# Kernel optimization log

Measured on AMD Instinct MI355X. Metric: run time of the kernel, lower is better.

The kernel has to match this reference:

```python
import jax, jax.numpy as jnp
import numpy as np
from jax import lax

DN3D = ('NCDHW', 'OIDHW', 'NCDHW')


def conv4d_valid(x, w, b):
    """4D valid convolution, stride 1.
    x: [B, C, L, D, H, W]; w: [O, C, Lk, Dk, Hk, Wk]; b: [O].
    Implemented as a small fixed loop over the Lk kernel positions, each a
    batched 3D conv (L folded into batch) -- same math as torch Conv4d above.
    """
    B, C, L, D, H, W = x.shape
    O, _, Lk, Dk, Hk, Wk = w.shape
    Lo = L - Lk + 1
    out = None
    for i in range(Lk):
        xs = x[:, :, i:i + Lo]                      # [B, C, Lo, D, H, W]
        xs = xs.transpose(0, 2, 1, 3, 4, 5).reshape(B * Lo, C, D, H, W)
        o = lax.conv_general_dilated(xs, w[:, :, i], (1, 1, 1), 'VALID',
                                     dimension_numbers=DN3D)  # [B*Lo, O, Do, Ho, Wo]
        out = o if out is None else out + o
    _, _, Do, Ho, Wo = out.shape
    out = out.reshape(B, Lo, O, Do, Ho, Wo).transpose(0, 2, 1, 3, 4, 5)
    return out + b[None, :, None, None, None, None]


def setup_inputs() -> dict:
    key = jax.random.key(0)
    k0, k1, k2, k3, k4 = jax.random.split(key, 5)
    B = 16384
    return {
        'x': jax.random.normal(k0, (B, 1, 7, 7, 7, 7), dtype=jnp.float32),
        'w1': jax.random.normal(k1, (2, 1, 3, 3, 3, 3), dtype=jnp.float32) * 0.1,
        'b1': jax.random.normal(k2, (2,), dtype=jnp.float32) * 0.1,
        'w2': jax.random.normal(k3, (4, 2, 3, 3, 3, 3), dtype=jnp.float32) * 0.1,
        'b2': jax.random.normal(k4, (4,), dtype=jnp.float32) * 0.1,
    }


def reference(x, w1, b1, w2, b2):
    h = jax.nn.relu(conv4d_valid(x, w1, b1))   # [B, 2, 5, 5, 5, 5]
    h = jax.nn.relu(conv4d_valid(h, w2, b2))   # [B, 4, 3, 3, 3, 3]
    return h.reshape(h.shape[0], -1)           # [B, 324]
```

## Files before the change

### kernel.cpp

```cpp
#include <hip/hip_runtime.h>

#define SPB 4
#define TPB 256

__global__ __launch_bounds__(TPB, 2)
void conv4d_fused(const float* __restrict__ x,
                  const float* __restrict__ w1, const float* __restrict__ b1,
                  const float* __restrict__ w2, const float* __restrict__ b2,
                  float* __restrict__ out, int B)
{
    __shared__ float s_w1[162];
    __shared__ float s_w2[648];
    __shared__ float s_b1[2];
    __shared__ float s_b2[4];
    __shared__ float s_x[SPB * 2401];
    __shared__ float s_h1[SPB * 1250];

    const int t  = threadIdx.x;
    const int s0 = blockIdx.x * SPB;
    const int ns = min(SPB, B - s0);

    for (int i = t; i < 162; i += TPB) s_w1[i] = w1[i];
    for (int i = t; i < 648; i += TPB) s_w2[i] = w2[i];
    if (t < 2) s_b1[t] = b1[t];
    if (t < 4) s_b2[t] = b2[t];

    {
        const float* xp = x + (size_t)s0 * 2401;
        const int n = ns * 2401;
        for (int i = t; i < n; i += TPB) s_x[i] = xp[i];
    }
    __syncthreads();

    {
        const int ntask = ns * 50;
        if (t < ntask) {
            int s = t / 50;
            int r = t % 50;
            int o = r / 25; r %= 25;
            int l = r / 5, d = r % 5;

            float acc[5][5];
            const float bias = s_b1[o];
            #pragma unroll
            for (int h = 0; h < 5; ++h)
                #pragma unroll
                for (int w = 0; w < 5; ++w) acc[h][w] = bias;

            const float* xs = s_x + s * 2401;
            const float* wo = s_w1 + o * 81;
            #pragma unroll
            for (int kl = 0; kl < 3; ++kl)
            #pragma unroll
            for (int kd = 0; kd < 3; ++kd) {
                float p[7][7];
                const float* xp = xs + (l + kl) * 343 + (d + kd) * 49;
                #pragma unroll
                for (int i = 0; i < 49; ++i) p[i / 7][i % 7] = xp[i];
                const float* wp = wo + kl * 27 + kd * 9;
                #pragma unroll
                for (int kh = 0; kh < 3; ++kh)
                #pragma unroll
                for (int kw = 0; kw < 3; ++kw) {
                    const float wv = wp[kh * 3 + kw];
                    #pragma unroll
                    for (int h = 0; h < 5; ++h)
                    #pragma unroll
                    for (int w = 0; w < 5; ++w)
                        acc[h][w] += p[h + kh][w + kw] * wv;
                }
            }
            float* hp = s_h1 + s * 1250 + o * 625 + l * 125 + d * 25;
            #pragma unroll
            for (int h = 0; h < 5; ++h)
            #pragma unroll
            for (int w = 0; w < 5; ++w)
                hp[h * 5 + w] = fmaxf(acc[h][w], 0.0f);
        }
    }
    __syncthreads();

    {
        const int ntask = ns * 36;
        if (t < ntask) {
            int s = t / 36;
            int r = t % 36;
            int o2 = r / 9; r %= 9;
            int l = r / 3, d = r % 3;

            float acc[3][3];
            const float bias = s_b2[o2];
            #pragma unroll
            for (int h = 0; h < 3; ++h)
                #pragma unroll
                for (int w = 0; w < 3; ++w) acc[h][w] = bias;

            #pragma unroll
            for (int c = 0; c < 2; ++c) {
                const float* hs = s_h1 + s * 1250 + c * 625;
                const float* wb = s_w2 + o2 * 162 + c * 81;
                #pragma unroll
                for (int kl = 0; kl < 3; ++kl)
                #pragma unroll
                for (int kd = 0; kd < 3; ++kd) {
                    float p[5][5];
                    const float* pp = hs + (l + kl) * 125 + (d + kd) * 25;
                    #pragma unroll
                    for (int i = 0; i < 25; ++i) p[i / 5][i % 5] = pp[i];
                    const float* wp = wb + kl * 27 + kd * 9;
                    #pragma unroll
                    for (int kh = 0; kh < 3; ++kh)
                    #pragma unroll
                    for (int kw = 0; kw < 3; ++kw) {
                        const float wv = wp[kh * 3 + kw];
                        #pragma unroll
                        for (int h = 0; h < 3; ++h)
                        #pragma unroll
                        for (int w = 0; w < 3; ++w)
                            acc[h][w] += p[h + kh][w + kw] * wv;
                    }
                }
            }
            float* op = out + (size_t)(s0 + s) * 324 + o2 * 81 + l * 27 + d * 9;
            #pragma unroll
            for (int h = 0; h < 3; ++h)
            #pragma unroll
            for (int w = 0; w < 3; ++w)
                op[h * 3 + w] = fmaxf(acc[h][w], 0.0f);
        }
    }
}

extern "C" void kernel_launch(void* const* d_in, const int* in_sizes, int n_in,
                              void* d_out, int out_size, void* d_ws, size_t ws_size,
                              hipStream_t stream)
{
    const float* x  = (const float*)d_in[0];
    const float* w1 = (const float*)d_in[1];
    const float* b1 = (const float*)d_in[2];
    const float* w2 = (const float*)d_in[3];
    const float* b2 = (const float*)d_in[4];
    float* out = (float*)d_out;

    const int B = in_sizes[0] / 2401;
    const int grid = (B + SPB - 1) / SPB;
    conv4d_fused<<<grid, TPB, 0, stream>>>(x, w1, b1, w2, b2, out, B);
}
```

Before: 314.4 us.

## Pack input and intermediate in bf16 in LDS with vectorized padded loads

Input planes and the layer-1 activations are now rounded to bf16 and stored two per 32-bit word in shared memory. Each plane is padded so it can be read with 128-bit loads, and the weights are padded for float4 loads. Samples per block rise to five and the occupancy hint goes from 2 to 3 blocks per SM, so LDS traffic and footprint drop. In exchange, input and intermediate values lose precision to bf16, which may break a strict accuracy tolerance, and the unpack step adds ALU work.

New measurement: 383.0 us. 21.8% more time.

```diff
diff --git a/kernel.cpp b/kernel.cpp
--- a/kernel.cpp
+++ b/kernel.cpp
@@ -1,132 +1,187 @@
 #include <hip/hip_runtime.h>
 
-#define SPB 4
+#define SPB 5
 #define TPB 256
 
-__global__ __launch_bounds__(TPB, 2)
+
+__device__ __forceinline__ unsigned bf16rne(float f) {
+    unsigned u = __float_as_uint(f);
+    return (u + 0x7fffu + ((u >> 16) & 1u)) >> 16;
+}
+__device__ __forceinline__ void unpack2(unsigned u, float& a, float& b) {
+    a = __uint_as_float(u << 16);
+    b = __uint_as_float(u & 0xffff0000u);
+}
+
+__global__ __launch_bounds__(TPB, 3)
 void conv4d_fused(const float* __restrict__ x,
                   const float* __restrict__ w1, const float* __restrict__ b1,
                   const float* __restrict__ w2, const float* __restrict__ b2,
                   float* __restrict__ out, int B)
 {
-    __shared__ float s_w1[162];
-    __shared__ float s_w2[648];
+    __shared__ __align__(16) unsigned s_xu[SPB * 49 * 28];
+    __shared__ __align__(16) unsigned s_h1[SPB * 2 * 25 * 16];
+    __shared__ __align__(16) float s_w1[18 * 12];
+    __shared__ __align__(16) float s_w2[72 * 12];
     __shared__ float s_b1[2];
     __shared__ float s_b2[4];
-    __shared__ float s_x[SPB * 2401];
-    __shared__ float s_h1[SPB * 1250];
 
     const int t  = threadIdx.x;
     const int s0 = blockIdx.x * SPB;
     const int ns = min(SPB, B - s0);
 
-    for (int i = t; i < 162; i += TPB) s_w1[i] = w1[i];
-    for (int i = t; i < 648; i += TPB) s_w2[i] = w2[i];
+    for (int i = t; i < 162; i += TPB) { int p = i / 9, q = i % 9; s_w1[p * 12 + q] = w1[i]; }
+    for (int i = t; i < 648; i += TPB) { int p = i / 9, q = i % 9; s_w2[p * 12 + q] = w2[i]; }
     if (t < 2) s_b1[t] = b1[t];
     if (t < 4) s_b2[t] = b2[t];
 
     {
-        const float* xp = x + (size_t)s0 * 2401;
-        const int n = ns * 2401;
-        for (int i = t; i < n; i += TPB) s_x[i] = xp[i];
-    }
-    __syncthreads();
-
-    {
-        const int ntask = ns * 50;
-        if (t < ntask) {
-            int s = t / 50;
-            int r = t % 50;
-            int o = r / 25; r %= 25;
-            int l = r / 5, d = r % 5;
-
-            float acc[5][5];
-            const float bias = s_b1[o];
-            #pragma unroll
-            for (int h = 0; h < 5; ++h)
-                #pragma unroll
-                for (int w = 0; w < 5; ++w) acc[h][w] = bias;
-
-            const float* xs = s_x + s * 2401;
-            const float* wo = s_w1 + o * 81;
-            #pragma unroll
-            for (int kl = 0; kl < 3; ++kl)
-            #pragma unroll
-            for (int kd = 0; kd < 3; ++kd) {
-                float p[7][7];
-                const float* xp = xs + (l + kl) * 343 + (d + kd) * 49;
-                #pragma unroll
-                for (int i = 0; i < 49; ++i) p[i / 7][i % 7] = xp[i];
-                const float* wp = wo + kl * 27 + kd * 9;
-                #pragma unroll
-                for (int kh = 0; kh < 3; ++kh)
-                #pragma unroll
-                for (int kw = 0; kw < 3; ++kw) {
-                    const float wv = wp[kh * 3 + kw];
-                    #pragma unroll
-                    for (int h = 0; h < 5; ++h)
-                    #pragma unroll
-                    for (int w = 0; w < 5; ++w)
-                        acc[h][w] += p[h + kh][w + kw] * wv;
-                }
-            }
-            float* hp = s_h1 + s * 1250 + o * 625 + l * 125 + d * 25;
-            #pragma unroll
-            for (int h = 0; h < 5; ++h)
-            #pragma unroll
-            for (int w = 0; w < 5; ++w)
-                hp[h * 5 + w] = fmaxf(acc[h][w], 0.0f);
+        const int nunits = ns * 49 * 25;
+        for (int u = t; u < nunits; u += TPB) {
+            int s = u / 1225;
+            int r = u % 1225;
+            int p = r / 25;
+            int j = r % 25;
+            const float* gp = x + (size_t)(s0 + s) * 2401 + p * 49;
+            unsigned* lp = s_xu + s * 1372 + p * 28;
+            if (j < 24) {
+                float a = gp[2 * j], b = gp[2 * j + 1];
+                lp[j] = bf16rne(a) | (bf16rne(b) << 16);
+            } else {
+                lp[24] = bf16rne(gp[48]);
+            }
         }
     }
     __syncthreads();
 
-    {
-        const int ntask = ns * 36;
-        if (t < ntask) {
-            int s = t / 36;
-            int r = t % 36;
-            int o2 = r / 9; r %= 9;
-            int l = r / 3, d = r % 3;
-
-            float acc[3][3];
+    if (t < 250) {
+        int o = t / 125;
+        int r = t % 125;
+        int s = r / 25;
+        int ld = r % 25;
+        int l = ld / 5, d = ld % 5;
+        if (s < ns) {
+            float acc[25];
+            const float bias = s_b1[o];
+            #pragma unroll
+            for (int i = 0; i < 25; ++i) acc[i] = bias;
+
+            const unsigned* xb = s_xu + s * 1372 + (l * 7 + d) * 28;
+            const float* wb = s_w1 + o * 108;
+
+            #pragma unroll
+            for (int kl = 0; kl < 3; ++kl)
+            #pragma unroll
+            for (int kd = 0; kd < 3; ++kd) {
+                const unsigned* pp = xb + (kl * 7 + kd) * 28;
+                unsigned u[25];
+                #pragma unroll
+                for (int q4 = 0; q4 < 6; ++q4) {
+                    uint4 q = ((const uint4*)pp)[q4];
+                    u[q4 * 4 + 0] = q.x; u[q4 * 4 + 1] = q.y;
+                    u[q4 * 4 + 2] = q.z; u[q4 * 4 + 3] = q.w;
+                }
+                u[24] = pp[24];
+                float X[49];
+                #pragma unroll
+                for (int i = 0; i < 24; ++i) unpack2(u[i], X[2 * i], X[2 * i + 1]);
+                X[48] = __uint_as_float(u[24] << 16);
+
+                const float* wp = wb + (kl * 3 + kd) * 12;
+                float wv[9];
+                float4 wq0 = *(const float4*)wp;
+                float4 wq1 = *(const float4*)(wp + 4);
+                wv[0] = wq0.x; wv[1] = wq0.y; wv[2] = wq0.z; wv[3] = wq0.w;
+                wv[4] = wq1.x; wv[5] = wq1.y; wv[6] = wq1.z; wv[7] = wq1.w;
+                wv[8] = wp[8];
+
+                #pragma unroll
+                for (int kh = 0; kh < 3; ++kh)
+                #pragma unroll
+                for (int kw = 0; kw < 3; ++kw) {
+                    const float wvv = wv[kh * 3 + kw];
+                    #pragma unroll
+                    for (int h = 0; h < 5; ++h)
+                    #pragma unroll
+                    for (int w = 0; w < 5; ++w)
+                        acc[h * 5 + w] += X[(h + kh) * 7 + (w + kw)] * wvv;
+                }
+            }
+
+            unsigned* hp = s_h1 + ((s * 2 + o) * 25 + ld) * 16;
+            unsigned pk[12];
+            #pragma unroll
+            for (int j = 0; j < 12; ++j) {
+                float a = fmaxf(acc[2 * j], 0.0f);
+                float b = fmaxf(acc[2 * j + 1], 0.0f);
+                pk[j] = bf16rne(a) | (bf16rne(b) << 16);
+            }
+            ((uint4*)hp)[0] = make_uint4(pk[0], pk[1], pk[2], pk[3]);
+            ((uint4*)hp)[1] = make_uint4(pk[4], pk[5], pk[6], pk[7]);
+            ((uint4*)hp)[2] = make_uint4(pk[8], pk[9], pk[10], pk[11]);
+            hp[12] = bf16rne(fmaxf(acc[24], 0.0f));
+        }
+    }
+    __syncthreads();
+
+    if (t < 180) {
+        int s = t / 36;
+        int r = t % 36;
+        int o2 = r / 9;
+        int ld = r % 9;
+        int l = ld / 3, d = ld % 3;
+        if (s < ns) {
+            float acc[9];
             const float bias = s_b2[o2];
             #pragma unroll
-            for (int h = 0; h < 3; ++h)
-                #pragma unroll
-                for (int w = 0; w < 3; ++w) acc[h][w] = bias;
+            for (int i = 0; i < 9; ++i) acc[i] = bias;
 
             #pragma unroll
             for (int c = 0; c < 2; ++c) {
-                const float* hs = s_h1 + s * 1250 + c * 625;
-                const float* wb = s_w2 + o2 * 162 + c * 81;
+                const unsigned* hb = s_h1 + ((s * 2 + c) * 25 + (l * 5 + d)) * 16;
+                const float* wb = s_w2 + ((o2 * 2 + c) * 9) * 12;
                 #pragma unroll
                 for (int kl = 0; kl < 3; ++kl)
                 #pragma unroll
                 for (int kd = 0; kd < 3; ++kd) {
-                    float p[5][5];
-                    const float* pp = hs + (l + kl) * 125 + (d + kd) * 25;
-                    #pragma unroll
-                    for (int i = 0; i < 25; ++i) p[i / 5][i % 5] = pp[i];
-                    const float* wp = wb + kl * 27 + kd * 9;
+                    const unsigned* pp = hb + (kl * 5 + kd) * 16;
+                    unsigned u[13];
+                    #pragma unroll
+                    for (int q4 = 0; q4 < 3; ++q4) {
+                        uint4 q = ((const uint4*)pp)[q4];
+                        u[q4 * 4 + 0] = q.x; u[q4 * 4 + 1] = q.y;
+                        u[q4 * 4 + 2] = q.z; u[q4 * 4 + 3] = q.w;
+                    }
+                    u[12] = pp[12];
+                    float X[25];
+                    #pragma unroll
+                    for (int i = 0; i < 12; ++i) unpack2(u[i], X[2 * i], X[2 * i + 1]);
+                    X[24] = __uint_as_float(u[12] << 16);
+
+                    const float* wp = wb + (kl * 3 + kd) * 12;
+                    float wv[9];
+                    float4 wq0 = *(const float4*)wp;
+                    float4 wq1 = *(const float4*)(wp + 4);
+                    wv[0] = wq0.x; wv[1] = wq0.y; wv[2] = wq0.z; wv[3] = wq0.w;
+                    wv[4] = wq1.x; wv[5] = wq1.y; wv[6] = wq1.z; wv[7] = wq1.w;
+                    wv[8] = wp[8];
+
                     #pragma unroll
                     for (int kh = 0; kh < 3; ++kh)
                     #pragma unroll
                     for (int kw = 0; kw < 3; ++kw) {
-                        const float wv = wp[kh * 3 + kw];
+                        const float wvv = wv[kh * 3 + kw];
                         #pragma unroll
                         for (int h = 0; h < 3; ++h)
                         #pragma unroll
                         for (int w = 0; w < 3; ++w)
-                            acc[h][w] += p[h + kh][w + kw] * wv;
+                            acc[h * 3 + w] += X[(h + kh) * 5 + (w + kw)] * wvv;
                     }
                 }
             }
             float* op = out + (size_t)(s0 + s) * 324 + o2 * 81 + l * 27 + d * 9;
             #pragma unroll
-            for (int h = 0; h < 3; ++h)
-            #pragma unroll
-            for (int w = 0; w < 3; ++w)
-                op[h * 3 + w] = fmaxf(acc[h][w], 0.0f);
+            for (int i = 0; i < 9; ++i) op[i] = fmaxf(acc[i], 0.0f);
         }
     }
 }
```

## Store input and intermediate activations as packed bf16 in LDS, fuse output channels

Applied to the files above, without the earlier changes.

Input planes and the first-layer activations are converted to bf16 and packed two per 32-bit word in shared memory, with padded strides, so more samples fit per block (SPB raised from 4 to 9) and LDS reads can be vectorised. Each first-layer thread now computes both output channels and each second-layer thread all four, so every loaded plane is reused across channels. Weights are re-laid-out for float4 loads. This lowers precision of the intermediates to bf16, which may exceed the accuracy tolerance, and uses more registers per thread.

Result: slower. 435.3 us (+38.5%).

```diff
diff --git a/kernel.cpp b/kernel.cpp
--- a/kernel.cpp
+++ b/kernel.cpp
@@ -1,7 +1,21 @@
 #include <hip/hip_runtime.h>
 
-#define SPB 4
 #define TPB 256
+#define SPB 9
+#define XSTRIDE 1396
+#define HSTRIDE 700
+
+__device__ __forceinline__ unsigned bf16rne(float f) {
+    unsigned u = __float_as_uint(f);
+    return (u + 0x7fffu + ((u >> 16) & 1u)) >> 16;
+}
+__device__ __forceinline__ void unpack2(unsigned u, float& a, float& b) {
+    a = __uint_as_float(u << 16);
+    b = __uint_as_float(u & 0xffff0000u);
+}
+__device__ __forceinline__ int xplane(int p) {
+    return 28 * p + (((p >> 3) & 7) << 2);
+}
 
 __global__ __launch_bounds__(TPB, 2)
 void conv4d_fused(const float* __restrict__ x,
@@ -9,124 +23,193 @@
                   const float* __restrict__ w2, const float* __restrict__ b2,
                   float* __restrict__ out, int B)
 {
-    __shared__ float s_w1[162];
-    __shared__ float s_w2[648];
-    __shared__ float s_b1[2];
-    __shared__ float s_b2[4];
-    __shared__ float s_x[SPB * 2401];
-    __shared__ float s_h1[SPB * 1250];
+    __shared__ __align__(16) unsigned s_xu[SPB * XSTRIDE];
+    __shared__ __align__(16) unsigned s_h1[SPB * HSTRIDE];
+    __shared__ __align__(16) float s_w1[9 * 2 * 12];
+    __shared__ __align__(16) float s_w2[2 * 9 * 4 * 12];
 
     const int t  = threadIdx.x;
     const int s0 = blockIdx.x * SPB;
-    const int ns = min(SPB, B - s0);
-
-    for (int i = t; i < 162; i += TPB) s_w1[i] = w1[i];
-    for (int i = t; i < 648; i += TPB) s_w2[i] = w2[i];
-    if (t < 2) s_b1[t] = b1[t];
-    if (t < 4) s_b2[t] = b2[t];
-
-    {
-        const float* xp = x + (size_t)s0 * 2401;
-        const int n = ns * 2401;
-        for (int i = t; i < n; i += TPB) s_x[i] = xp[i];
+
+    for (int i = t; i < 162; i += TPB) {
+        int o = i / 81, r = i - o * 81;
+        int klkd = r / 9, tap = r - klkd * 9;
+        s_w1[(klkd * 2 + o) * 12 + tap] = w1[i];
+    }
+    for (int i = t; i < 648; i += TPB) {
+        int o2 = i / 162, r = i - o2 * 162;
+        int c = r / 81, r2 = r - c * 81;
+        int klkd = r2 / 9, tap = r2 - klkd * 9;
+        s_w2[((c * 9 + klkd) * 4 + o2) * 12 + tap] = w2[i];
+    }
+
+    for (int s = 0; s < SPB; ++s) {
+        if (s0 + s >= B) break;
+        const float* gx = x + (size_t)(s0 + s) * 2401;
+        unsigned* xw = s_xu + s * XSTRIDE;
+        for (int i = t; i < 1225; i += TPB) {
+            int p = i / 25;
+            int j = i - p * 25;
+            const float* gp = gx + p * 49 + 2 * j;
+            float a = gp[0];
+            float b = (j < 24) ? gp[1] : 0.0f;
+            xw[xplane(p) + j] = bf16rne(a) | (bf16rne(b) << 16);
+        }
     }
     __syncthreads();
 
-    {
-        const int ntask = ns * 50;
-        if (t < ntask) {
-            int s = t / 50;
-            int r = t % 50;
-            int o = r / 25; r %= 25;
-            int l = r / 5, d = r % 5;
-
-            float acc[5][5];
-            const float bias = s_b1[o];
-            #pragma unroll
-            for (int h = 0; h < 5; ++h)
-                #pragma unroll
-                for (int w = 0; w < 5; ++w) acc[h][w] = bias;
-
-            const float* xs = s_x + s * 2401;
-            const float* wo = s_w1 + o * 81;
+    if (t < SPB * 25) {
+        int s  = t / 25;
+        int ld = t - s * 25;
+        if (s0 + s < B) {
+            int l = ld / 5, d = ld - (ld / 5) * 5;
+            float acc0[25], acc1[25];
+            const float bb0 = b1[0], bb1 = b1[1];
+            #pragma unroll
+            for (int i = 0; i < 25; ++i) { acc0[i] = bb0; acc1[i] = bb1; }
+
+            const unsigned* xw = s_xu + s * XSTRIDE;
+            const int pbase = l * 7 + d;
             #pragma unroll
             for (int kl = 0; kl < 3; ++kl)
             #pragma unroll
             for (int kd = 0; kd < 3; ++kd) {
-                float p[7][7];
-                const float* xp = xs + (l + kl) * 343 + (d + kd) * 49;
-                #pragma unroll
-                for (int i = 0; i < 49; ++i) p[i / 7][i % 7] = xp[i];
-                const float* wp = wo + kl * 27 + kd * 9;
+                const int p = pbase + kl * 7 + kd;
+                const unsigned* pp = xw + xplane(p);
+                unsigned u[25];
+                #pragma unroll
+                for (int k = 0; k < 6; ++k) {
+                    uint4 q = ((const uint4*)pp)[k];
+                    u[4*k] = q.x; u[4*k+1] = q.y; u[4*k+2] = q.z; u[4*k+3] = q.w;
+                }
+                u[24] = pp[24];
+                float X[50];
+                #pragma unroll
+                for (int k = 0; k < 25; ++k) unpack2(u[k], X[2*k], X[2*k+1]);
+
+                const float* wp = s_w1 + (kl * 3 + kd) * 24;
+                float wv0[9], wv1[9];
+                {
+                    float4 A = *(const float4*)wp;
+                    float4 Bq = *(const float4*)(wp + 4);
+                    wv0[0]=A.x; wv0[1]=A.y; wv0[2]=A.z; wv0[3]=A.w;
+                    wv0[4]=Bq.x; wv0[5]=Bq.y; wv0[6]=Bq.z; wv0[7]=Bq.w;
+                    wv0[8]=wp[8];
+                    float4 C = *(const float4*)(wp + 12);
+                    float4 Dq = *(const float4*)(wp + 16);
+                    wv1[0]=C.x; wv1[1]=C.y; wv1[2]=C.z; wv1[3]=C.w;
+                    wv1[4]=Dq.x; wv1[5]=Dq.y; wv1[6]=Dq.z; wv1[7]=Dq.w;
+                    wv1[8]=wp[20];
+                }
+
                 #pragma unroll
                 for (int kh = 0; kh < 3; ++kh)
                 #pragma unroll
                 for (int kw = 0; kw < 3; ++kw) {
-                    const float wv = wp[kh * 3 + kw];
+                    const float w0v = wv0[kh*3+kw], w1v = wv1[kh*3+kw];
                     #pragma unroll
                     for (int h = 0; h < 5; ++h)
                     #pragma unroll
-                    for (int w = 0; w < 5; ++w)
-                        acc[h][w] += p[h + kh][w + kw] * wv;
+                    for (int w = 0; w < 5; ++w) {
+                        const float xv = X[(h+kh)*7 + (w+kw)];
+                        acc0[h*5+w] += xv * w0v;
+                        acc1[h*5+w] += xv * w1v;
+                    }
                 }
             }
-            float* hp = s_h1 + s * 1250 + o * 625 + l * 125 + d * 25;
-            #pragma unroll
-            for (int h = 0; h < 5; ++h)
-            #pragma unroll
-            for (int w = 0; w < 5; ++w)
-                hp[h * 5 + w] = fmaxf(acc[h][w], 0.0f);
+
+            unsigned* hp0 = s_h1 + s * HSTRIDE + 14 * ld;
+            unsigned* hp1 = hp0 + 14 * 25;
+            unsigned pk[13];
+            #pragma unroll
+            for (int k = 0; k < 12; ++k)
+                pk[k] = bf16rne(fmaxf(acc0[2*k],0.f)) | (bf16rne(fmaxf(acc0[2*k+1],0.f)) << 16);
+            pk[12] = bf16rne(fmaxf(acc0[24],0.f));
+            #pragma unroll
+            for (int k = 0; k < 6; ++k) ((uint2*)hp0)[k] = make_uint2(pk[2*k], pk[2*k+1]);
+            hp0[12] = pk[12];
+            #pragma unroll
+            for (int k = 0; k < 12; ++k)
+                pk[k] = bf16rne(fmaxf(acc1[2*k],0.f)) | (bf16rne(fmaxf(acc1[2*k+1],0.f)) << 16);
+            pk[12] = bf16rne(fmaxf(acc1[24],0.f));
+            #pragma unroll
+            for (int k = 0; k < 6; ++k) ((uint2*)hp1)[k] = make_uint2(pk[2*k], pk[2*k+1]);
+            hp1[12] = pk[12];
         }
     }
     __syncthreads();
 
-    {
-        const int ntask = ns * 36;
-        if (t < ntask) {
-            int s = t / 36;
-            int r = t % 36;
-            int o2 = r / 9; r %= 9;
-            int l = r / 3, d = r % 3;
-
-            float acc[3][3];
-            const float bias = s_b2[o2];
-            #pragma unroll
-            for (int h = 0; h < 3; ++h)
-                #pragma unroll
-                for (int w = 0; w < 3; ++w) acc[h][w] = bias;
-
-            #pragma unroll
-            for (int c = 0; c < 2; ++c) {
-                const float* hs = s_h1 + s * 1250 + c * 625;
-                const float* wb = s_w2 + o2 * 162 + c * 81;
-                #pragma unroll
-                for (int kl = 0; kl < 3; ++kl)
-                #pragma unroll
-                for (int kd = 0; kd < 3; ++kd) {
-                    float p[5][5];
-                    const float* pp = hs + (l + kl) * 125 + (d + kd) * 25;
-                    #pragma unroll
-                    for (int i = 0; i < 25; ++i) p[i / 5][i % 5] = pp[i];
-                    const float* wp = wb + kl * 27 + kd * 9;
-                    #pragma unroll
-                    for (int kh = 0; kh < 3; ++kh)
-                    #pragma unroll
-                    for (int kw = 0; kw < 3; ++kw) {
-                        const float wv = wp[kh * 3 + kw];
-                        #pragma unroll
-                        for (int h = 0; h < 3; ++h)
-                        #pragma unroll
-                        for (int w = 0; w < 3; ++w)
-                            acc[h][w] += p[h + kh][w + kw] * wv;
+    if (t < SPB * 9) {
+        int s  = t / 9;
+        int ld = t - s * 9;
+        if (s0 + s < B) {
+            int l = ld / 3, d = ld - (ld / 3) * 3;
+            float acc[4][9];
+            #pragma unroll
+            for (int o2 = 0; o2 < 4; ++o2) {
+                const float bb = b2[o2];
+                #pragma unroll
+                for (int i = 0; i < 9; ++i) acc[o2][i] = bb;
+            }
+
+            const unsigned* hw = s_h1 + s * HSTRIDE;
+            const int qbase = l * 5 + d;
+            #pragma unroll
+            for (int c = 0; c < 2; ++c)
+            #pragma unroll
+            for (int kl = 0; kl < 3; ++kl)
+            #pragma unroll
+            for (int kd = 0; kd < 3; ++kd) {
+                const int q = c * 25 + qbase + kl * 5 + kd;
+                const unsigned* pp = hw + 14 * q;
+                unsigned u[13];
+                #pragma unroll
+                for (int k = 0; k < 6; ++k) {
+                    uint2 qq = ((const uint2*)pp)[k];
+                    u[2*k] = qq.x; u[2*k+1] = qq.y;
+                }
+                u[12] = pp[12];
+                float X[26];
+                #pragma unroll
+                for (int k = 0; k < 13; ++k) unpack2(u[k], X[2*k], X[2*k+1]);
+
+                const float* wp = s_w2 + (c * 9 + (kl*3+kd)) * 48;
+                float wv[4][9];
+                #pragma unroll
+                for (int o2 = 0; o2 < 4; ++o2) {
+                    const float* wq = wp + o2 * 12;
+                    float4 A = *(const float4*)wq;
+                    float4 Bq = *(const float4*)(wq + 4);
+                    wv[o2][0]=A.x; wv[o2][1]=A.y; wv[o2][2]=A.z; wv[o2][3]=A.w;
+                    wv[o2][4]=Bq.x; wv[o2][5]=Bq.y; wv[o2][6]=Bq.z; wv[o2][7]=Bq.w;
+                    wv[o2][8]=wq[8];
+                }
+
+                #pragma unroll
+                for (int kh = 0; kh < 3; ++kh)
+                #pragma unroll
+                for (int kw = 0; kw < 3; ++kw) {
+                    const float w0v = wv[0][kh*3+kw], w1v = wv[1][kh*3+kw];
+                    const float w2v = wv[2][kh*3+kw], w3v = wv[3][kh*3+kw];
+                    #pragma unroll
+                    for (int h = 0; h < 3; ++h)
+                    #pragma unroll
+                    for (int w = 0; w < 3; ++w) {
+                        const float xv = X[(h+kh)*5 + (w+kw)];
+                        acc[0][h*3+w] += xv * w0v;
+                        acc[1][h*3+w] += xv * w1v;
+                        acc[2][h*3+w] += xv * w2v;
+                        acc[3][h*3+w] += xv * w3v;
                     }
                 }
             }
-            float* op = out + (size_t)(s0 + s) * 324 + o2 * 81 + l * 27 + d * 9;
-            #pragma unroll
-            for (int h = 0; h < 3; ++h)
-            #pragma unroll
-            for (int w = 0; w < 3; ++w)
-                op[h * 3 + w] = fmaxf(acc[h][w], 0.0f);
+
+            float* op = out + (size_t)(s0 + s) * 324 + ld * 9;
+            #pragma unroll
+            for (int o2 = 0; o2 < 4; ++o2)
+                #pragma unroll
+                for (int i = 0; i < 9; ++i)
+                    op[o2 * 81 + i] = fmaxf(acc[o2][i], 0.f);
         }
     }
 }
```

## Convert fused conv4d to packed fp16 math with reorganized shared layouts

Applied to the files above, without the earlier changes.

Inputs, weights and intermediate activations are converted to packed half2 in shared memory with padded, vector-aligned row layouts. Both conv stages then use packed fp16 FMAs and 128-bit LDS loads. Stage 1 computes both output channels per thread, and stage 2 packs the two input channels into half2 lanes and splits output channels across thread pairs. Samples per block rise from 4 to 9. This is meant to halve ALU and LDS traffic per FMA, at the cost of fp16 precision for accumulation, which may exceed the tolerance.

New measurement: 369.8 us. +17.6%, slower.

```diff
diff --git a/kernel.cpp b/kernel.cpp
--- a/kernel.cpp
+++ b/kernel.cpp
@@ -1,7 +1,19 @@
 #include <hip/hip_runtime.h>
-
-#define SPB 4
+#include <hip/hip_fp16.h>
+
 #define TPB 256
+#define SPB 9
+#define XS  1372
+#define HS  700
+
+__device__ __forceinline__ unsigned h2u(__half2 h) { return __builtin_bit_cast(unsigned, h); }
+__device__ __forceinline__ __half2 u2h(unsigned u) { return __builtin_bit_cast(__half2, u); }
+__device__ __forceinline__ unsigned pkf(float a, float b) { return h2u(__floats2half2_rn(a, b)); }
+__device__ __forceinline__ unsigned pkrelu(unsigned u) {
+    unsigned r;
+    __asm__ volatile("v_pk_max_f16 %0, %1, 0" : "=v"(r) : "v"(u));
+    return r;
+}
 
 __global__ __launch_bounds__(TPB, 2)
 void conv4d_fused(const float* __restrict__ x,
@@ -9,124 +21,189 @@
                   const float* __restrict__ w2, const float* __restrict__ b2,
                   float* __restrict__ out, int B)
 {
-    __shared__ float s_w1[162];
-    __shared__ float s_w2[648];
-    __shared__ float s_b1[2];
+    __shared__ __align__(16) unsigned s_x[SPB * XS];
+    __shared__ __align__(16) unsigned s_h[SPB * HS];
+    __shared__ __align__(16) unsigned s_w1d[216];
+    __shared__ __align__(16) unsigned s_w2d[432];
+    __shared__ unsigned s_b1d[2];
     __shared__ float s_b2[4];
-    __shared__ float s_x[SPB * 2401];
-    __shared__ float s_h1[SPB * 1250];
 
     const int t  = threadIdx.x;
     const int s0 = blockIdx.x * SPB;
     const int ns = min(SPB, B - s0);
 
-    for (int i = t; i < 162; i += TPB) s_w1[i] = w1[i];
-    for (int i = t; i < 648; i += TPB) s_w2[i] = w2[i];
-    if (t < 2) s_b1[t] = b1[t];
+    for (int i = t; i < 162; i += TPB) {
+        int o = i / 81, r81 = i - 81 * o;
+        int klkd = r81 / 9, t9 = r81 - 9 * klkd;
+        float v = w1[i];
+        s_w1d[((klkd * 2 + o) * 12) + t9] = pkf(v, v);
+    }
+    for (int i = t; i < 324; i += TPB) {
+        int o2 = i / 81, r81 = i - 81 * o2;
+        int klkd = r81 / 9, t9 = r81 - 9 * klkd;
+        s_w2d[((klkd * 4 + o2) * 12) + t9] = pkf(w2[o2 * 162 + r81], w2[o2 * 162 + 81 + r81]);
+    }
+    if (t < 2) { float v = b1[t]; s_b1d[t] = pkf(v, v); }
     if (t < 4) s_b2[t] = b2[t];
 
     {
-        const float* xp = x + (size_t)s0 * 2401;
-        const int n = ns * 2401;
-        for (int i = t; i < n; i += TPB) s_x[i] = xp[i];
+        const int nunit = ns * XS;
+        for (int v = t; v < nunit; v += TPB) {
+            int s  = v / XS;     int r0 = v - s * XS;
+            int p  = r0 / 28;    int r1 = r0 - p * 28;
+            int r  = r1 >> 2, c = r1 & 3;
+            const float* gp = x + (size_t)(s0 + s) * 2401 + p * 49 + r * 7;
+            float a = gp[c < 3 ? 2 * c : 6];
+            float b = (c < 3) ? gp[2 * c + 1] : 0.0f;
+            s_x[v] = pkf(a, b);
+        }
     }
     __syncthreads();
 
-    {
-        const int ntask = ns * 50;
-        if (t < ntask) {
-            int s = t / 50;
-            int r = t % 50;
-            int o = r / 25; r %= 25;
-            int l = r / 5, d = r % 5;
-
-            float acc[5][5];
-            const float bias = s_b1[o];
-            #pragma unroll
-            for (int h = 0; h < 5; ++h)
-                #pragma unroll
-                for (int w = 0; w < 5; ++w) acc[h][w] = bias;
-
-            const float* xs = s_x + s * 2401;
-            const float* wo = s_w1 + o * 81;
+    if (t < SPB * 25) {
+        int s = t / 25, ld = t - 25 * s;
+        if (s < ns) {
+            int l = ld / 5, d = ld - 5 * l;
+            __half2 acc[2][5][3];
+            {
+                __half2 bb0 = u2h(s_b1d[0]), bb1 = u2h(s_b1d[1]);
+                #pragma unroll
+                for (int h = 0; h < 5; ++h)
+                    #pragma unroll
+                    for (int j = 0; j < 3; ++j) { acc[0][h][j] = bb0; acc[1][h][j] = bb1; }
+            }
+            const unsigned* xb = s_x + s * XS + (l * 7 + d) * 28;
+
             #pragma unroll
             for (int kl = 0; kl < 3; ++kl)
             #pragma unroll
             for (int kd = 0; kd < 3; ++kd) {
-                float p[7][7];
-                const float* xp = xs + (l + kl) * 343 + (d + kd) * 49;
-                #pragma unroll
-                for (int i = 0; i < 49; ++i) p[i / 7][i % 7] = xp[i];
-                const float* wp = wo + kl * 27 + kd * 9;
+                const unsigned* pp = xb + (kl * 7 + kd) * 28;
+                unsigned e[7][4];
+                #pragma unroll
+                for (int r = 0; r < 7; ++r) {
+                    uint4 q = ((const uint4*)pp)[r];
+                    e[r][0] = q.x; e[r][1] = q.y; e[r][2] = q.z; e[r][3] = q.w;
+                }
+                unsigned od[7][3];
+                #pragma unroll
+                for (int r = 0; r < 7; ++r)
+                    #pragma unroll
+                    for (int j = 0; j < 3; ++j)
+                        od[r][j] = __builtin_amdgcn_alignbit(e[r][j + 1], e[r][j], 16);
+
+                unsigned wv[2][9];
+                #pragma unroll
+                for (int o = 0; o < 2; ++o) {
+                    const unsigned* wb = s_w1d + ((kl * 3 + kd) * 2 + o) * 12;
+                    uint4 qa = ((const uint4*)wb)[0];
+                    uint4 qb = ((const uint4*)wb)[1];
+                    wv[o][0] = qa.x; wv[o][1] = qa.y; wv[o][2] = qa.z; wv[o][3] = qa.w;
+                    wv[o][4] = qb.x; wv[o][5] = qb.y; wv[o][6] = qb.z; wv[o][7] = qb.w;
+                    wv[o][8] = wb[8];
+                }
+
                 #pragma unroll
                 for (int kh = 0; kh < 3; ++kh)
                 #pragma unroll
-                for (int kw = 0; kw < 3; ++kw) {
-                    const float wv = wp[kh * 3 + kw];
-                    #pragma unroll
-                    for (int h = 0; h < 5; ++h)
-                    #pragma unroll
-                    for (int w = 0; w < 5; ++w)
-                        acc[h][w] += p[h + kh][w + kw] * wv;
-                }
-            }
-            float* hp = s_h1 + s * 1250 + o * 625 + l * 125 + d * 25;
-            #pragma unroll
-            for (int h = 0; h < 5; ++h)
-            #pragma unroll
-            for (int w = 0; w < 5; ++w)
-                hp[h * 5 + w] = fmaxf(acc[h][w], 0.0f);
+                for (int h = 0; h < 5; ++h) {
+                    const int row = h + kh;
+                    #pragma unroll
+                    for (int kw = 0; kw < 3; ++kw) {
+                        #pragma unroll
+                        for (int j = 0; j < 3; ++j) {
+                            unsigned xu = (kw == 0) ? e[row][j]
+                                        : (kw == 1) ? od[row][j]
+                                                    : e[row][j + 1];
+                            __half2 X2 = u2h(xu);
+                            acc[0][h][j] = __hfma2(X2, u2h(wv[0][kh * 3 + kw]), acc[0][h][j]);
+                            acc[1][h][j] = __hfma2(X2, u2h(wv[1][kh * 3 + kw]), acc[1][h][j]);
+                        }
+                    }
+                }
+            }
+
+            unsigned* hp = s_h + s * HS + ld * 28;
+            unsigned o25[25];
+            #pragma unroll
+            for (int h = 0; h < 5; ++h) {
+                unsigned c0[3], c1[3];
+                #pragma unroll
+                for (int j = 0; j < 3; ++j) {
+                    c0[j] = pkrelu(h2u(acc[0][h][j]));
+                    c1[j] = pkrelu(h2u(acc[1][h][j]));
+                }
+                o25[h * 5 + 0] = __builtin_amdgcn_perm(c1[0], c0[0], 0x05040100u);
+                o25[h * 5 + 1] = __builtin_amdgcn_perm(c1[0], c0[0], 0x07060302u);
+                o25[h * 5 + 2] = __builtin_amdgcn_perm(c1[1], c0[1], 0x05040100u);
+                o25[h * 5 + 3] = __builtin_amdgcn_perm(c1[1], c0[1], 0x07060302u);
+                o25[h * 5 + 4] = __builtin_amdgcn_perm(c1[2], c0[2], 0x05040100u);
+            }
+            #pragma unroll
+            for (int k = 0; k < 6; ++k)
+                ((uint4*)hp)[k] = make_uint4(o25[4 * k], o25[4 * k + 1], o25[4 * k + 2], o25[4 * k + 3]);
+            hp[24] = o25[24];
         }
     }
     __syncthreads();
 
-    {
-        const int ntask = ns * 36;
-        if (t < ntask) {
-            int s = t / 36;
-            int r = t % 36;
-            int o2 = r / 9; r %= 9;
-            int l = r / 3, d = r % 3;
-
-            float acc[3][3];
-            const float bias = s_b2[o2];
-            #pragma unroll
-            for (int h = 0; h < 3; ++h)
-                #pragma unroll
-                for (int w = 0; w < 3; ++w) acc[h][w] = bias;
-
-            #pragma unroll
-            for (int c = 0; c < 2; ++c) {
-                const float* hs = s_h1 + s * 1250 + c * 625;
-                const float* wb = s_w2 + o2 * 162 + c * 81;
-                #pragma unroll
-                for (int kl = 0; kl < 3; ++kl)
-                #pragma unroll
-                for (int kd = 0; kd < 3; ++kd) {
-                    float p[5][5];
-                    const float* pp = hs + (l + kl) * 125 + (d + kd) * 25;
-                    #pragma unroll
-                    for (int i = 0; i < 25; ++i) p[i / 5][i % 5] = pp[i];
-                    const float* wp = wb + kl * 27 + kd * 9;
+    if (t < SPB * 18) {
+        int q = t >> 1, o2p = t & 1;
+        int s = q / 9, ld = q - 9 * s;
+        if (s < ns) {
+            int l = ld / 3, d = ld - 3 * l;
+            __half2 acc[2][9];
+            #pragma unroll
+            for (int j = 0; j < 2; ++j)
+                #pragma unroll
+                for (int i = 0; i < 9; ++i) acc[j][i] = u2h(0u);
+
+            const unsigned* hb = s_h + s * HS + (l * 5 + d) * 28;
+            #pragma unroll
+            for (int kl = 0; kl < 3; ++kl)
+            #pragma unroll
+            for (int kd = 0; kd < 3; ++kd) {
+                const unsigned* pp = hb + (kl * 5 + kd) * 28;
+                unsigned u[25];
+                #pragma unroll
+                for (int k = 0; k < 6; ++k) {
+                    uint4 qq = ((const uint4*)pp)[k];
+                    u[4*k] = qq.x; u[4*k+1] = qq.y; u[4*k+2] = qq.z; u[4*k+3] = qq.w;
+                }
+                u[24] = pp[24];
+
+                #pragma unroll
+                for (int j = 0; j < 2; ++j) {
+                    const int o2 = 2 * o2p + j;
+                    const unsigned* wb = s_w2d + ((kl * 3 + kd) * 4 + o2) * 12;
+                    uint4 qa = ((const uint4*)wb)[0];
+                    uint4 qb = ((const uint4*)wb)[1];
+                    unsigned wv[9] = {qa.x, qa.y, qa.z, qa.w, qb.x, qb.y, qb.z, qb.w, wb[8]};
                     #pragma unroll
                     for (int kh = 0; kh < 3; ++kh)
                     #pragma unroll
                     for (int kw = 0; kw < 3; ++kw) {
-                        const float wv = wp[kh * 3 + kw];
+                        __half2 W2 = u2h(wv[kh * 3 + kw]);
                         #pragma unroll
                         for (int h = 0; h < 3; ++h)
                         #pragma unroll
                         for (int w = 0; w < 3; ++w)
-                            acc[h][w] += p[h + kh][w + kw] * wv;
+                            acc[j][h * 3 + w] =
+                                __hfma2(u2h(u[(h + kh) * 5 + (w + kw)]), W2, acc[j][h * 3 + w]);
                     }
                 }
             }
-            float* op = out + (size_t)(s0 + s) * 324 + o2 * 81 + l * 27 + d * 9;
-            #pragma unroll
-            for (int h = 0; h < 3; ++h)
-            #pragma unroll
-            for (int w = 0; w < 3; ++w)
-                op[h * 3 + w] = fmaxf(acc[h][w], 0.0f);
+
+            float* op = out + (size_t)(s0 + s) * 324 + o2p * 162 + ld * 9;
+            #pragma unroll
+            for (int j = 0; j < 2; ++j) {
+                const float bb = s_b2[2 * o2p + j];
+                #pragma unroll
+                for (int i = 0; i < 9; ++i) {
+                    float v = __low2float(acc[j][i]) + __high2float(acc[j][i]) + bb;
+                    op[j * 81 + i] = fmaxf(v, 0.0f);
+                }
+            }
         }
     }
 }
```
